# Optimization experiments

Hardware: AMD Instinct MI355X
Metric: run time of the kernel (lower is better)

The kernel has to match this reference:

```python
import jax, jax.numpy as jnp
import numpy as np

B, H, W, F, D = 8, 126, 126, 64, 32
ITERS, NIT = 3, 20
RHO, NU, DT, FRC = 1.0, 0.1, 0.1, 1.0
DX = 2.0 / (B + 1)
DY = 2.0 / (H + 1)
DX2, DY2 = DX * DX, DY * DY
DEN = 2.0 * (DX2 + DY2)


def _b_term(du_dx, dv_dy, du_dy, dv_dx):
    return RHO * ((du_dx + dv_dy) / DT - du_dx**2 - 2.0 * du_dy * dv_dx - dv_dy**2)


def build_b(u, v):
    b = jnp.zeros_like(u)
    # interior
    b = b.at[:, 1:-1, 1:-1].set(_b_term(
        (u[:, 1:-1, 2:] - u[:, 1:-1, :-2]) / (2 * DX),
        (v[:, 2:, 1:-1] - v[:, :-2, 1:-1]) / (2 * DY),
        (u[:, 2:, 1:-1] - u[:, :-2, 1:-1]) / (2 * DY),
        (v[:, 1:-1, 2:] - v[:, 1:-1, :-2]) / (2 * DX)))
    # periodic wrap, last column
    b = b.at[:, 1:-1, -1].set(_b_term(
        (u[:, 1:-1, 0] - u[:, 1:-1, -2]) / (2 * DX),
        (v[:, 2:, -1] - v[:, :-2, -1]) / (2 * DY),
        (u[:, 2:, -1] - u[:, :-2, -1]) / (2 * DY),
        (v[:, 1:-1, 0] - v[:, 1:-1, -2]) / (2 * DX)))
    # periodic wrap, first column
    b = b.at[:, 1:-1, 0].set(_b_term(
        (u[:, 1:-1, 1] - u[:, 1:-1, -1]) / (2 * DX),
        (v[:, 2:, 0] - v[:, :-2, 0]) / (2 * DY),
        (u[:, 2:, 0] - u[:, :-2, 0]) / (2 * DY),
        (v[:, 1:-1, 1] - v[:, 1:-1, -1]) / (2 * DX)))
    return b


def pressure_poisson(p, b):
    c = DX2 * DY2 / DEN

    def step(p, _):
        pn = p
        p = p.at[:, 1:-1, 1:-1].set(
            ((pn[:, 1:-1, 2:] + pn[:, 1:-1, :-2]) * DY2 + (pn[:, 2:, 1:-1] + pn[:, :-2, 1:-1]) * DX2) / DEN
            - c * b[:, 1:-1, 1:-1])
        p = p.at[:, 1:-1, -1].set(
            ((pn[:, 1:-1, 0] + pn[:, 1:-1, -2]) * DY2 + (pn[:, 2:, -1] + pn[:, :-2, -1]) * DX2) / DEN
            - c * b[:, 1:-1, -1])
        p = p.at[:, 1:-1, 0].set(
            ((pn[:, 1:-1, 1] + pn[:, 1:-1, -1]) * DY2 + (pn[:, 2:, 0] + pn[:, :-2, 0]) * DX2) / DEN
            - c * b[:, 1:-1, 0])
        # Neumann-style row boundaries (copy from updated p, as in torch code)
        p = p.at[:, -1].set(p[:, -2])
        p = p.at[:, 0].set(p[:, 1])
        return p, None

    p, _ = jax.lax.scan(step, p, None, length=NIT)
    return p


def velocity_step(u, v, p):
    un, vn = u, v
    uc = un[:, 1:-1, 1:-1]
    vc = vn[:, 1:-1, 1:-1]
    u_i = (uc - uc * DT / DX * (uc - un[:, 1:-1, :-2]) - vc * DT / DY * (uc - un[:, :-2, 1:-1])
           - DT / (2 * RHO * DX) * (p[:, 1:-1, 2:] - p[:, 1:-1, :-2])
           + NU * (DT / DX2 * (un[:, 1:-1, 2:] - 2 * uc + un[:, 1:-1, :-2])
                   + DT / DY2 * (un[:, 2:, 1:-1] - 2 * uc + un[:, :-2, 1:-1]))
           + FRC * DT)
    v_i = (vc - uc * DT / DX * (vc - vn[:, 1:-1, :-2]) - vc * DT / DY * (vc - vn[:, :-2, 1:-1])
           - DT / (2 * RHO * DY) * (p[:, 2:, 1:-1] - p[:, :-2, 1:-1])
           + NU * (DT / DX2 * (vn[:, 1:-1, 2:] - 2 * vc + vn[:, 1:-1, :-2])
                   + DT / DY2 * (vn[:, 2:, 1:-1] - 2 * vc + vn[:, :-2, 1:-1])))
    ue = un[:, 1:-1, -1]
    ve = vn[:, 1:-1, -1]
    u_e = (ue - ue * DT / DX * (ue - un[:, 1:-1, -2]) - ve * DT / DY * (ue - un[:, :-2, -1])
           - DT / (2 * RHO * DX) * (p[:, 1:-1, 0] - p[:, 1:-1, -2])
           + NU * (DT / DX2 * (un[:, 1:-1, 0] - 2 * ue + un[:, 1:-1, -2])
                   + DT / DY2 * (un[:, 2:, -1] - 2 * ue + un[:, :-2, -1]))
           + FRC * DT)
    v_e = (ve - ue * DT / DX * (ve - vn[:, 1:-1, -2]) - ve * DT / DY * (ve - vn[:, :-2, -1])
           - DT / (2 * RHO * DY) * (p[:, 2:, -1] - p[:, :-2, -1])
           + NU * (DT / DX2 * (vn[:, 1:-1, 0] - 2 * ve + vn[:, 1:-1, -2])
                   + DT / DY2 * (vn[:, 2:, -1] - 2 * ve + vn[:, :-2, -1])))
    u0c = un[:, 1:-1, 0]
    v0c = vn[:, 1:-1, 0]
    u_0 = (u0c - u0c * DT / DX * (u0c - un[:, 1:-1, -1]) - v0c * DT / DY * (u0c - un[:, :-2, 0])
           - DT / (2 * RHO * DX) * (p[:, 1:-1, 1] - p[:, 1:-1, -1])
           + NU * (DT / DX2 * (un[:, 1:-1, 1] - 2 * u0c + un[:, 1:-1, -1])
                   + DT / DY2 * (un[:, 2:, 0] - 2 * u0c + un[:, :-2, 0]))
           + FRC * DT)
    v_0 = (v0c - u0c * DT / DX * (v0c - vn[:, 1:-1, -1]) - v0c * DT / DY * (v0c - vn[:, :-2, 0])
           - DT / (2 * RHO * DY) * (p[:, 2:, 0] - p[:, :-2, 0])
           + NU * (DT / DX2 * (vn[:, 1:-1, 1] - 2 * v0c + vn[:, 1:-1, -1])
                   + DT / DY2 * (vn[:, 2:, 0] - 2 * v0c + vn[:, :-2, 0])))
    u = un.at[:, 1:-1, 1:-1].set(u_i).at[:, 1:-1, -1].set(u_e).at[:, 1:-1, 0].set(u_0)
    v = vn.at[:, 1:-1, 1:-1].set(v_i).at[:, 1:-1, -1].set(v_e).at[:, 1:-1, 0].set(v_0)
    u = u.at[:, 0].set(0.0).at[:, -1].set(0.0)
    v = v.at[:, 0].set(0.0).at[:, -1].set(0.0)
    return u, v


def setup_inputs() -> dict:
    key = jax.random.key(0)
    ks = jax.random.split(key, 5)
    x = jax.random.normal(ks[0], (B, H, W, F), jnp.float32) * 0.05
    u0 = jax.random.normal(ks[1], (B, H + 2, W + 2, D), jnp.float32) * 0.05
    v0 = jax.random.normal(ks[2], (B, H + 2, W + 2, D), jnp.float32) * 0.05
    w = jax.random.normal(ks[3], (D, F), jnp.float32) / np.float32(np.sqrt(F))
    b_lin = jax.random.normal(ks[4], (D,), jnp.float32) * 0.01
    return {"x": x, "u0": u0, "v0": v0, "w": w, "b_lin": b_lin}


def reference(x, u0, v0, w, b_lin):
    # pad spatial dims by 1 then linear preprocess: (B,H+2,W+2,F) -> (B,H+2,W+2,D)
    p = jnp.pad(x, ((0, 0), (1, 1), (1, 1), (0, 0)))
    p = jnp.einsum('bhwf,df->bhwd', p, w) + b_lin
    u, v = u0, v0
    for _ in range(ITERS):
        b = build_b(u, v)
        p = pressure_poisson(p, b)
        u, v = velocity_step(u, v, p)
    return p[:, -1, :, :]  # (B, W+2, D)
```

## Files before the change

### kernel.cpp

```cpp
#include <hip/hip_runtime.h>

#define NITER 20
#define OUTER 3

constexpr double DXd  = 2.0 / 9.0;
constexpr double DYd  = 2.0 / 127.0;
constexpr double DX2d = DXd * DXd;
constexpr double DY2d = DYd * DYd;
constexpr double DENd = 2.0 * (DX2d + DY2d);

constexpr float K1     = (float)(DY2d / DENd);
constexpr float K2     = (float)(DX2d / DENd);
constexpr float CC     = (float)(DX2d * DY2d / DENd);
constexpr float INV2DX = (float)(1.0 / (2.0 * DXd));
constexpr float INV2DY = (float)(1.0 / (2.0 * DYd));
constexpr float INVDT  = (float)(1.0 / 0.1);
constexpr float DTDX   = (float)(0.1 / DXd);
constexpr float DTDY   = (float)(0.1 / DYd);
constexpr float PGX    = (float)(0.1 / (2.0 * 1.0 * DXd));
constexpr float PGY    = (float)(0.1 / (2.0 * 1.0 * DYd));
constexpr float A1     = (float)(0.1 / DX2d);
constexpr float A2     = (float)(0.1 / DY2d);
constexpr float NUf    = 0.1f;
constexpr float FDT    = 0.1f;

__device__ __forceinline__ float bperm(int srcByte, float v) {
    return __int_as_float(__builtin_amdgcn_ds_bpermute(srcByte, __float_as_int(v)));
}

__global__ __launch_bounds__(256) void einsum_kernel(
    const float* __restrict__ x, const float* __restrict__ w,
    const float* __restrict__ bl, float* __restrict__ p0)
{
    int id = blockIdx.x * 256 + threadIdx.x;
    int c = id & 127, r = (id >> 7) & 127, b = id >> 14;
    float acc[32];
#pragma unroll
    for (int d = 0; d < 32; ++d) acc[d] = bl[d];
    if (r >= 1 && r <= 126 && c >= 1 && c <= 126) {
        const float* xp = x + (((size_t)(b * 126 + (r - 1))) * 126 + (c - 1)) * 64;
#pragma unroll
        for (int f = 0; f < 64; f += 4) {
            float4 xv = *(const float4*)(xp + f);
#pragma unroll
            for (int d = 0; d < 32; ++d) {
                acc[d] += xv.x * w[d * 64 + f] + xv.y * w[d * 64 + f + 1]
                        + xv.z * w[d * 64 + f + 2] + xv.w * w[d * 64 + f + 3];
            }
        }
    }
    float* op = p0 + ((size_t)b * 32) * 16384 + r * 128 + c;
#pragma unroll
    for (int d = 0; d < 32; ++d) op[(size_t)d * 16384] = acc[d];
}

__global__ __launch_bounds__(512, 2) void sim_kernel(
    const float* __restrict__ u0, const float* __restrict__ v0,
    const float* __restrict__ p0ws, const float* __restrict__ x,
    const float* __restrict__ w, const float* __restrict__ bl,
    float* __restrict__ out, int use_ws)
{
    __shared__ float sP[2][16][2][128];
    __shared__ float sU[16][2][128];
    __shared__ float sV[16][2][128];

    const int tid = threadIdx.x;
    const int tx = tid & 31, ty = tid >> 5;
    const int c0 = tx << 2, r0 = ty << 3;
    const int lane = tid & 63;
    const int srcL = (((lane & 32) | ((lane + 31) & 31)) << 2);
    const int srcR = (((lane & 32) | ((lane + 1) & 31)) << 2);
    const int bb = blockIdx.x & 7;
    const int d  = blockIdx.x >> 3;

    float pC[8][4], uC[8][4], vC[8][4], cb[8][4];

#pragma unroll
    for (int r = 0; r < 8; ++r) {
        const size_t base = ((size_t)((bb * 128 + (r0 + r)) * 128 + c0)) * 32 + d;
#pragma unroll
        for (int c = 0; c < 4; ++c) {
            uC[r][c] = u0[base + (size_t)c * 32];
            vC[r][c] = v0[base + (size_t)c * 32];
        }
    }

    if (use_ws) {
        const float* pp = p0ws + ((size_t)(bb * 32 + d)) * 16384;
#pragma unroll
        for (int r = 0; r < 8; ++r) {
            float4 t = *(const float4*)(pp + (r0 + r) * 128 + c0);
            pC[r][0] = t.x; pC[r][1] = t.y; pC[r][2] = t.z; pC[r][3] = t.w;
        }
    } else {
        const float blv = bl[d];
#pragma unroll
        for (int r = 0; r < 8; ++r) {
            const int gr = r0 + r;
#pragma unroll
            for (int c = 0; c < 4; ++c) {
                const int gc = c0 + c;
                float acc = blv;
                if (gr >= 1 && gr <= 126 && gc >= 1 && gc <= 126) {
                    const float* xp = x + (((size_t)(bb * 126 + (gr - 1))) * 126 + (gc - 1)) * 64;
                    for (int f = 0; f < 64; f += 4) {
                        float4 xv = *(const float4*)(xp + f);
                        acc += xv.x * w[d * 64 + f] + xv.y * w[d * 64 + f + 1]
                             + xv.z * w[d * 64 + f + 2] + xv.w * w[d * 64 + f + 3];
                    }
                }
                pC[r][c] = acc;
            }
        }
    }

    int s = 0;
    *(float4*)&sP[0][ty][0][c0] = make_float4(pC[0][0], pC[0][1], pC[0][2], pC[0][3]);
    *(float4*)&sP[0][ty][1][c0] = make_float4(pC[7][0], pC[7][1], pC[7][2], pC[7][3]);
    *(float4*)&sU[ty][0][c0]    = make_float4(uC[0][0], uC[0][1], uC[0][2], uC[0][3]);
    *(float4*)&sU[ty][1][c0]    = make_float4(uC[7][0], uC[7][1], uC[7][2], uC[7][3]);
    *(float4*)&sV[ty][0][c0]    = make_float4(vC[0][0], vC[0][1], vC[0][2], vC[0][3]);
    *(float4*)&sV[ty][1][c0]    = make_float4(vC[7][0], vC[7][1], vC[7][2], vC[7][3]);
    __syncthreads();

    const int tyN = (ty > 0) ? ty - 1 : 0;
    const int tyS = (ty < 15) ? ty + 1 : 15;

    for (int outer = 0; outer < OUTER; ++outer) {
        {
            float4 uN4 = *(const float4*)&sU[tyN][1][c0];
            float4 uS4 = *(const float4*)&sU[tyS][0][c0];
            float4 vN4 = *(const float4*)&sV[tyN][1][c0];
            float4 vS4 = *(const float4*)&sV[tyS][0][c0];
            float uNh[4] = {uN4.x, uN4.y, uN4.z, uN4.w};
            float uSh[4] = {uS4.x, uS4.y, uS4.z, uS4.w};
            float vNh[4] = {vN4.x, vN4.y, vN4.z, vN4.w};
            float vSh[4] = {vS4.x, vS4.y, vS4.z, vS4.w};
#pragma unroll
            for (int r = 0; r < 8; ++r) {
                const int gr = r0 + r;
                const bool valid = (gr >= 1) && (gr <= 126);
                float uWh = bperm(srcL, uC[r][3]);
                float uEh = bperm(srcR, uC[r][0]);
                float vWh = bperm(srcL, vC[r][3]);
                float vEh = bperm(srcR, vC[r][0]);
#pragma unroll
                for (int c = 0; c < 4; ++c) {
                    float uE = (c < 3) ? uC[r][c + 1] : uEh;
                    float uW = (c > 0) ? uC[r][c - 1] : uWh;
                    float vE = (c < 3) ? vC[r][c + 1] : vEh;
                    float vW = (c > 0) ? vC[r][c - 1] : vWh;
                    float uN = (r > 0) ? uC[r - 1][c] : uNh[c];
                    float uS = (r < 7) ? uC[r + 1][c] : uSh[c];
                    float vN = (r > 0) ? vC[r - 1][c] : vNh[c];
                    float vS = (r < 7) ? vC[r + 1][c] : vSh[c];
                    float dudx = (uE - uW) * INV2DX;
                    float dvdy = (vS - vN) * INV2DY;
                    float dudy = (uS - uN) * INV2DY;
                    float dvdx = (vE - vW) * INV2DX;
                    float bt = (dudx + dvdy) * INVDT - dudx * dudx
                             - 2.0f * dudy * dvdx - dvdy * dvdy;
                    cb[r][c] = valid ? CC * bt : 0.0f;
                }
            }
        }

        for (int it = 0; it < NITER; ++it) {
            float4 t4 = *(const float4*)&sP[s][tyN][1][c0];
            float4 b4 = *(const float4*)&sP[s][tyS][0][c0];
            float nrow[4] = {t4.x, t4.y, t4.z, t4.w};
            float shalo[4] = {b4.x, b4.y, b4.z, b4.w};
#pragma unroll
            for (int r = 0; r < 8; ++r) {
                const int gr = r0 + r;
                const bool valid = (gr >= 1) && (gr <= 126);
                float old0[4];
#pragma unroll
                for (int c = 0; c < 4; ++c) old0[c] = pC[r][c];
                float pWh = bperm(srcL, old0[3]);
                float pEh = bperm(srcR, old0[0]);
#pragma unroll
                for (int c = 0; c < 4; ++c) {
                    float E = (c < 3) ? old0[c + 1] : pEh;
                    float W = (c > 0) ? old0[c - 1] : pWh;
                    float N = nrow[c];
                    float S = (r < 7) ? pC[r + 1][c] : shalo[c];
                    float nv = (E + W) * K1 + (N + S) * K2 - cb[r][c];
                    pC[r][c] = valid ? nv : old0[c];
                }
#pragma unroll
                for (int c = 0; c < 4; ++c) nrow[c] = old0[c];
            }
            if (ty == 0) {
#pragma unroll
                for (int c = 0; c < 4; ++c) pC[0][c] = pC[1][c];
            }
            if (ty == 15) {
#pragma unroll
                for (int c = 0; c < 4; ++c) pC[7][c] = pC[6][c];
            }
            *(float4*)&sP[s ^ 1][ty][0][c0] = make_float4(pC[0][0], pC[0][1], pC[0][2], pC[0][3]);
            *(float4*)&sP[s ^ 1][ty][1][c0] = make_float4(pC[7][0], pC[7][1], pC[7][2], pC[7][3]);
            __syncthreads();
            s ^= 1;
        }

        {
            float4 ut4 = *(const float4*)&sU[tyN][1][c0];
            float4 us4 = *(const float4*)&sU[tyS][0][c0];
            float4 vt4 = *(const float4*)&sV[tyN][1][c0];
            float4 vs4 = *(const float4*)&sV[tyS][0][c0];
            float4 pt4 = *(const float4*)&sP[s][tyN][1][c0];
            float4 pb4 = *(const float4*)&sP[s][tyS][0][c0];
            float uNh[4] = {ut4.x, ut4.y, ut4.z, ut4.w};
            float uSh[4] = {us4.x, us4.y, us4.z, us4.w};
            float vNh[4] = {vt4.x, vt4.y, vt4.z, vt4.w};
            float vSh[4] = {vs4.x, vs4.y, vs4.z, vs4.w};
            float pNh[4] = {pt4.x, pt4.y, pt4.z, pt4.w};
            float pSh[4] = {pb4.x, pb4.y, pb4.z, pb4.w};
            __syncthreads();

            float uNrow[4], vNrow[4];
#pragma unroll
            for (int c = 0; c < 4; ++c) { uNrow[c] = uNh[c]; vNrow[c] = vNh[c]; }
#pragma unroll
            for (int r = 0; r < 8; ++r) {
                const int gr = r0 + r;
                const bool valid = (gr >= 1) && (gr <= 126);
                float uold[4], vold[4];
#pragma unroll
                for (int c = 0; c < 4; ++c) { uold[c] = uC[r][c]; vold[c] = vC[r][c]; }
                float uWh = bperm(srcL, uold[3]);
                float uEh = bperm(srcR, uold[0]);
                float vWh = bperm(srcL, vold[3]);
                float vEh = bperm(srcR, vold[0]);
                float pWh = bperm(srcL, pC[r][3]);
                float pEh = bperm(srcR, pC[r][0]);
#pragma unroll
                for (int c = 0; c < 4; ++c) {
                    float uc = uold[c], vc = vold[c];
                    float uE = (c < 3) ? uold[c + 1] : uEh;
                    float uW = (c > 0) ? uold[c - 1] : uWh;
                    float vE = (c < 3) ? vold[c + 1] : vEh;
                    float vW = (c > 0) ? vold[c - 1] : vWh;
                    float uN = uNrow[c];
                    float uS = (r < 7) ? uC[r + 1][c] : uSh[c];
                    float vN = vNrow[c];
                    float vS = (r < 7) ? vC[r + 1][c] : vSh[c];
                    float pE = (c < 3) ? pC[r][c + 1] : pEh;
                    float pW = (c > 0) ? pC[r][c - 1] : pWh;
                    float pN = (r > 0) ? pC[r - 1][c] : pNh[c];
                    float pS = (r < 7) ? pC[r + 1][c] : pSh[c];

                    float unew = uc - uc * DTDX * (uc - uW) - vc * DTDY * (uc - uN)
                               - PGX * (pE - pW)
                               + NUf * (A1 * (uE - 2.0f * uc + uW) + A2 * (uS - 2.0f * uc + uN))
                               + FDT;
                    float vnew = vc - uc * DTDX * (vc - vW) - vc * DTDY * (vc - vN)
                               - PGY * (pS - pN)
                               + NUf * (A1 * (vE - 2.0f * vc + vW) + A2 * (vS - 2.0f * vc + vN));
                    uC[r][c] = valid ? unew : uc;
                    vC[r][c] = valid ? vnew : vc;
                }
#pragma unroll
                for (int c = 0; c < 4; ++c) { uNrow[c] = uold[c]; vNrow[c] = vold[c]; }
            }
            if (ty == 0) {
#pragma unroll
                for (int c = 0; c < 4; ++c) { uC[0][c] = 0.0f; vC[0][c] = 0.0f; }
            }
            if (ty == 15) {
#pragma unroll
                for (int c = 0; c < 4; ++c) { uC[7][c] = 0.0f; vC[7][c] = 0.0f; }
            }
            *(float4*)&sU[ty][0][c0] = make_float4(uC[0][0], uC[0][1], uC[0][2], uC[0][3]);
            *(float4*)&sU[ty][1][c0] = make_float4(uC[7][0], uC[7][1], uC[7][2], uC[7][3]);
            *(float4*)&sV[ty][0][c0] = make_float4(vC[0][0], vC[0][1], vC[0][2], vC[0][3]);
            *(float4*)&sV[ty][1][c0] = make_float4(vC[7][0], vC[7][1], vC[7][2], vC[7][3]);
            __syncthreads();
        }
    }

    if (ty == 15) {
        float* op = out + ((size_t)bb * 128 + c0) * 32 + d;
        op[0]  = pC[7][0];
        op[32] = pC[7][1];
        op[64] = pC[7][2];
        op[96] = pC[7][3];
    }
}

extern "C" void kernel_launch(void* const* d_in, const int* in_sizes, int n_in,
                              void* d_out, int out_size, void* d_ws, size_t ws_size,
                              hipStream_t stream) {
    const float* x  = (const float*)d_in[0];
    const float* u0 = (const float*)d_in[1];
    const float* v0 = (const float*)d_in[2];
    const float* w  = (const float*)d_in[3];
    const float* bl = (const float*)d_in[4];
    float* out = (float*)d_out;
    float* p0  = (float*)d_ws;

    const size_t need = (size_t)8 * 32 * 128 * 128 * sizeof(float);
    const int use_ws = (ws_size >= need) ? 1 : 0;

    if (use_ws) {
        einsum_kernel<<<512, 256, 0, stream>>>(x, w, bl, p0);
    }
    sim_kernel<<<256, 512, 0, stream>>>(u0, v0, p0, x, w, bl, out, use_ws);
}
```

Baseline: 268.8 us.

## Double threads per block, halve rows per thread, skip final velocity update

Each block now runs 1024 threads, and each thread owns a 4x4 tile instead of 8x4. This raises the number of waves per CU and shortens each thread's serial dependency chain in the Jacobi sweeps. The separate P/U/V shared arrays become one reused buffer. The validity masks are dropped because boundary rows are overwritten anyway. The last outer iteration's velocity update is skipped since the output depends only on pressure. The trade-off is more threads at each barrier, extra syncs to reuse the shared buffer, and a relative increase in halo exchange traffic.

```diff
diff --git a/kernel.cpp b/kernel.cpp
--- a/kernel.cpp
+++ b/kernel.cpp
@@ -54,29 +54,29 @@
     for (int d = 0; d < 32; ++d) op[(size_t)d * 16384] = acc[d];
 }
 
-__global__ __launch_bounds__(512, 2) void sim_kernel(
+__global__ __launch_bounds__(1024, 4) void sim_kernel(
     const float* __restrict__ u0, const float* __restrict__ v0,
     const float* __restrict__ p0ws, const float* __restrict__ x,
     const float* __restrict__ w, const float* __restrict__ bl,
     float* __restrict__ out, int use_ws)
 {
-    __shared__ float sP[2][16][2][128];
-    __shared__ float sU[16][2][128];
-    __shared__ float sV[16][2][128];
+    __shared__ float S[32][4][128];
 
     const int tid = threadIdx.x;
     const int tx = tid & 31, ty = tid >> 5;
-    const int c0 = tx << 2, r0 = ty << 3;
+    const int c0 = tx << 2, r0 = ty << 2;
     const int lane = tid & 63;
     const int srcL = (((lane & 32) | ((lane + 31) & 31)) << 2);
     const int srcR = (((lane & 32) | ((lane + 1) & 31)) << 2);
     const int bb = blockIdx.x & 7;
     const int d  = blockIdx.x >> 3;
-
-    float pC[8][4], uC[8][4], vC[8][4], cb[8][4];
-
-#pragma unroll
-    for (int r = 0; r < 8; ++r) {
+    const int tyN = (ty > 0) ? ty - 1 : 0;
+    const int tyS = (ty < 31) ? ty + 1 : 31;
+
+    float pC[4][4], uC[4][4], vC[4][4], cb[4][4];
+
+#pragma unroll
+    for (int r = 0; r < 4; ++r) {
         const size_t base = ((size_t)((bb * 128 + (r0 + r)) * 128 + c0)) * 32 + d;
 #pragma unroll
         for (int c = 0; c < 4; ++c) {
@@ -88,14 +88,14 @@
     if (use_ws) {
         const float* pp = p0ws + ((size_t)(bb * 32 + d)) * 16384;
 #pragma unroll
-        for (int r = 0; r < 8; ++r) {
+        for (int r = 0; r < 4; ++r) {
             float4 t = *(const float4*)(pp + (r0 + r) * 128 + c0);
             pC[r][0] = t.x; pC[r][1] = t.y; pC[r][2] = t.z; pC[r][3] = t.w;
         }
     } else {
         const float blv = bl[d];
 #pragma unroll
-        for (int r = 0; r < 8; ++r) {
+        for (int r = 0; r < 4; ++r) {
             const int gr = r0 + r;
 #pragma unroll
             for (int c = 0; c < 4; ++c) {
@@ -114,79 +114,77 @@
         }
     }
 
-    int s = 0;
-    *(float4*)&sP[0][ty][0][c0] = make_float4(pC[0][0], pC[0][1], pC[0][2], pC[0][3]);
-    *(float4*)&sP[0][ty][1][c0] = make_float4(pC[7][0], pC[7][1], pC[7][2], pC[7][3]);
-    *(float4*)&sU[ty][0][c0]    = make_float4(uC[0][0], uC[0][1], uC[0][2], uC[0][3]);
-    *(float4*)&sU[ty][1][c0]    = make_float4(uC[7][0], uC[7][1], uC[7][2], uC[7][3]);
-    *(float4*)&sV[ty][0][c0]    = make_float4(vC[0][0], vC[0][1], vC[0][2], vC[0][3]);
-    *(float4*)&sV[ty][1][c0]    = make_float4(vC[7][0], vC[7][1], vC[7][2], vC[7][3]);
+    *(float4*)&S[ty][0][c0] = make_float4(uC[0][0], uC[0][1], uC[0][2], uC[0][3]);
+    *(float4*)&S[ty][1][c0] = make_float4(uC[3][0], uC[3][1], uC[3][2], uC[3][3]);
+    *(float4*)&S[ty][2][c0] = make_float4(vC[0][0], vC[0][1], vC[0][2], vC[0][3]);
+    *(float4*)&S[ty][3][c0] = make_float4(vC[3][0], vC[3][1], vC[3][2], vC[3][3]);
     __syncthreads();
 
-    const int tyN = (ty > 0) ? ty - 1 : 0;
-    const int tyS = (ty < 15) ? ty + 1 : 15;
-
     for (int outer = 0; outer < OUTER; ++outer) {
-        {
-            float4 uN4 = *(const float4*)&sU[tyN][1][c0];
-            float4 uS4 = *(const float4*)&sU[tyS][0][c0];
-            float4 vN4 = *(const float4*)&sV[tyN][1][c0];
-            float4 vS4 = *(const float4*)&sV[tyS][0][c0];
-            float uNh[4] = {uN4.x, uN4.y, uN4.z, uN4.w};
-            float uSh[4] = {uS4.x, uS4.y, uS4.z, uS4.w};
-            float vNh[4] = {vN4.x, vN4.y, vN4.z, vN4.w};
-            float vSh[4] = {vS4.x, vS4.y, vS4.z, vS4.w};
-#pragma unroll
-            for (int r = 0; r < 8; ++r) {
-                const int gr = r0 + r;
-                const bool valid = (gr >= 1) && (gr <= 126);
-                float uWh = bperm(srcL, uC[r][3]);
-                float uEh = bperm(srcR, uC[r][0]);
-                float vWh = bperm(srcL, vC[r][3]);
-                float vEh = bperm(srcR, vC[r][0]);
-#pragma unroll
-                for (int c = 0; c < 4; ++c) {
-                    float uE = (c < 3) ? uC[r][c + 1] : uEh;
-                    float uW = (c > 0) ? uC[r][c - 1] : uWh;
-                    float vE = (c < 3) ? vC[r][c + 1] : vEh;
-                    float vW = (c > 0) ? vC[r][c - 1] : vWh;
-                    float uN = (r > 0) ? uC[r - 1][c] : uNh[c];
-                    float uS = (r < 7) ? uC[r + 1][c] : uSh[c];
-                    float vN = (r > 0) ? vC[r - 1][c] : vNh[c];
-                    float vS = (r < 7) ? vC[r + 1][c] : vSh[c];
-                    float dudx = (uE - uW) * INV2DX;
-                    float dvdy = (vS - vN) * INV2DY;
-                    float dudy = (uS - uN) * INV2DY;
-                    float dvdx = (vE - vW) * INV2DX;
-                    float bt = (dudx + dvdy) * INVDT - dudx * dudx
-                             - 2.0f * dudy * dvdx - dvdy * dvdy;
-                    cb[r][c] = valid ? CC * bt : 0.0f;
-                }
-            }
-        }
+        float4 uN4 = *(const float4*)&S[tyN][1][c0];
+        float4 uS4 = *(const float4*)&S[tyS][0][c0];
+        float4 vN4 = *(const float4*)&S[tyN][3][c0];
+        float4 vS4 = *(const float4*)&S[tyS][2][c0];
+        float uNh[4] = {uN4.x, uN4.y, uN4.z, uN4.w};
+        float uSh[4] = {uS4.x, uS4.y, uS4.z, uS4.w};
+        float vNh[4] = {vN4.x, vN4.y, vN4.z, vN4.w};
+        float vSh[4] = {vS4.x, vS4.y, vS4.z, vS4.w};
+
+#pragma unroll
+        for (int r = 0; r < 4; ++r) {
+            float uWh = bperm(srcL, uC[r][3]);
+            float uEh = bperm(srcR, uC[r][0]);
+            float vWh = bperm(srcL, vC[r][3]);
+            float vEh = bperm(srcR, vC[r][0]);
+#pragma unroll
+            for (int c = 0; c < 4; ++c) {
+                float uE = (c < 3) ? uC[r][c + 1] : uEh;
+                float uW = (c > 0) ? uC[r][c - 1] : uWh;
+                float vE = (c < 3) ? vC[r][c + 1] : vEh;
+                float vW = (c > 0) ? vC[r][c - 1] : vWh;
+                float uN = (r > 0) ? uC[r - 1][c] : uNh[c];
+                float uS_ = (r < 3) ? uC[r + 1][c] : uSh[c];
+                float vN = (r > 0) ? vC[r - 1][c] : vNh[c];
+                float vS_ = (r < 3) ? vC[r + 1][c] : vSh[c];
+                float dudx = (uE - uW) * INV2DX;
+                float dvdy = (vS_ - vN) * INV2DY;
+                float dudy = (uS_ - uN) * INV2DY;
+                float dvdx = (vE - vW) * INV2DX;
+                float bt = (dudx + dvdy) * INVDT - dudx * dudx
+                         - 2.0f * dudy * dvdx - dvdy * dvdy;
+                cb[r][c] = CC * bt;
+            }
+        }
+        __syncthreads();
+        *(float4*)&S[ty][0][c0] = make_float4(pC[0][0], pC[0][1], pC[0][2], pC[0][3]);
+        *(float4*)&S[ty][1][c0] = make_float4(pC[3][0], pC[3][1], pC[3][2], pC[3][3]);
+        __syncthreads();
 
         for (int it = 0; it < NITER; ++it) {
-            float4 t4 = *(const float4*)&sP[s][tyN][1][c0];
-            float4 b4 = *(const float4*)&sP[s][tyS][0][c0];
+            const int rb = (it & 1) << 1;
+            const int wb = rb ^ 2;
+            float4 t4 = *(const float4*)&S[tyN][rb + 1][c0];
+            float4 b4 = *(const float4*)&S[tyS][rb + 0][c0];
             float nrow[4] = {t4.x, t4.y, t4.z, t4.w};
             float shalo[4] = {b4.x, b4.y, b4.z, b4.w};
-#pragma unroll
-            for (int r = 0; r < 8; ++r) {
-                const int gr = r0 + r;
-                const bool valid = (gr >= 1) && (gr <= 126);
+            float pWh[4], pEh[4];
+#pragma unroll
+            for (int r = 0; r < 4; ++r) {
+                pWh[r] = bperm(srcL, pC[r][3]);
+                pEh[r] = bperm(srcR, pC[r][0]);
+            }
+#pragma unroll
+            for (int r = 0; r < 4; ++r) {
                 float old0[4];
 #pragma unroll
                 for (int c = 0; c < 4; ++c) old0[c] = pC[r][c];
-                float pWh = bperm(srcL, old0[3]);
-                float pEh = bperm(srcR, old0[0]);
 #pragma unroll
                 for (int c = 0; c < 4; ++c) {
-                    float E = (c < 3) ? old0[c + 1] : pEh;
-                    float W = (c > 0) ? old0[c - 1] : pWh;
+                    float E = (c < 3) ? old0[c + 1] : pEh[r];
+                    float W = (c > 0) ? old0[c - 1] : pWh[r];
                     float N = nrow[c];
-                    float S = (r < 7) ? pC[r + 1][c] : shalo[c];
-                    float nv = (E + W) * K1 + (N + S) * K2 - cb[r][c];
-                    pC[r][c] = valid ? nv : old0[c];
+                    float Sv = (r < 3) ? pC[r + 1][c] : shalo[c];
+                    pC[r][c] = (E + W) * K1 + (N + Sv) * K2 - cb[r][c];
                 }
 #pragma unroll
                 for (int c = 0; c < 4; ++c) nrow[c] = old0[c];
@@ -195,38 +193,26 @@
 #pragma unroll
                 for (int c = 0; c < 4; ++c) pC[0][c] = pC[1][c];
             }
-            if (ty == 15) {
-#pragma unroll
-                for (int c = 0; c < 4; ++c) pC[7][c] = pC[6][c];
-            }
-            *(float4*)&sP[s ^ 1][ty][0][c0] = make_float4(pC[0][0], pC[0][1], pC[0][2], pC[0][3]);
-            *(float4*)&sP[s ^ 1][ty][1][c0] = make_float4(pC[7][0], pC[7][1], pC[7][2], pC[7][3]);
+            if (ty == 31) {
+#pragma unroll
+                for (int c = 0; c < 4; ++c) pC[3][c] = pC[2][c];
+            }
+            *(float4*)&S[ty][wb][c0]     = make_float4(pC[0][0], pC[0][1], pC[0][2], pC[0][3]);
+            *(float4*)&S[ty][wb + 1][c0] = make_float4(pC[3][0], pC[3][1], pC[3][2], pC[3][3]);
             __syncthreads();
-            s ^= 1;
-        }
-
-        {
-            float4 ut4 = *(const float4*)&sU[tyN][1][c0];
-            float4 us4 = *(const float4*)&sU[tyS][0][c0];
-            float4 vt4 = *(const float4*)&sV[tyN][1][c0];
-            float4 vs4 = *(const float4*)&sV[tyS][0][c0];
-            float4 pt4 = *(const float4*)&sP[s][tyN][1][c0];
-            float4 pb4 = *(const float4*)&sP[s][tyS][0][c0];
-            float uNh[4] = {ut4.x, ut4.y, ut4.z, ut4.w};
-            float uSh[4] = {us4.x, us4.y, us4.z, us4.w};
-            float vNh[4] = {vt4.x, vt4.y, vt4.z, vt4.w};
-            float vSh[4] = {vs4.x, vs4.y, vs4.z, vs4.w};
+        }
+
+        if (outer < OUTER - 1) {
+            float4 pt4 = *(const float4*)&S[tyN][1][c0];
+            float4 pb4 = *(const float4*)&S[tyS][0][c0];
             float pNh[4] = {pt4.x, pt4.y, pt4.z, pt4.w};
             float pSh[4] = {pb4.x, pb4.y, pb4.z, pb4.w};
-            __syncthreads();
 
             float uNrow[4], vNrow[4];
 #pragma unroll
             for (int c = 0; c < 4; ++c) { uNrow[c] = uNh[c]; vNrow[c] = vNh[c]; }
 #pragma unroll
-            for (int r = 0; r < 8; ++r) {
-                const int gr = r0 + r;
-                const bool valid = (gr >= 1) && (gr <= 126);
+            for (int r = 0; r < 4; ++r) {
                 float uold[4], vold[4];
 #pragma unroll
                 for (int c = 0; c < 4; ++c) { uold[c] = uC[r][c]; vold[c] = vC[r][c]; }
@@ -244,23 +230,23 @@
                     float vE = (c < 3) ? vold[c + 1] : vEh;
                     float vW = (c > 0) ? vold[c - 1] : vWh;
                     float uN = uNrow[c];
-                    float uS = (r < 7) ? uC[r + 1][c] : uSh[c];
+                    float uS_ = (r < 3) ? uC[r + 1][c] : uSh[c];
                     float vN = vNrow[c];
-                    float vS = (r < 7) ? vC[r + 1][c] : vSh[c];
+                    float vS_ = (r < 3) ? vC[r + 1][c] : vSh[c];
                     float pE = (c < 3) ? pC[r][c + 1] : pEh;
                     float pW = (c > 0) ? pC[r][c - 1] : pWh;
                     float pN = (r > 0) ? pC[r - 1][c] : pNh[c];
-                    float pS = (r < 7) ? pC[r + 1][c] : pSh[c];
+                    float pS = (r < 3) ? pC[r + 1][c] : pSh[c];
 
                     float unew = uc - uc * DTDX * (uc - uW) - vc * DTDY * (uc - uN)
                                - PGX * (pE - pW)
-                               + NUf * (A1 * (uE - 2.0f * uc + uW) + A2 * (uS - 2.0f * uc + uN))
+                               + NUf * (A1 * (uE - 2.0f * uc + uW) + A2 * (uS_ - 2.0f * uc + uN))
                                + FDT;
                     float vnew = vc - uc * DTDX * (vc - vW) - vc * DTDY * (vc - vN)
                                - PGY * (pS - pN)
-                               + NUf * (A1 * (vE - 2.0f * vc + vW) + A2 * (vS - 2.0f * vc + vN));
-                    uC[r][c] = valid ? unew : uc;
-                    vC[r][c] = valid ? vnew : vc;
+                               + NUf * (A1 * (vE - 2.0f * vc + vW) + A2 * (vS_ - 2.0f * vc + vN));
+                    uC[r][c] = unew;
+                    vC[r][c] = vnew;
                 }
 #pragma unroll
                 for (int c = 0; c < 4; ++c) { uNrow[c] = uold[c]; vNrow[c] = vold[c]; }
@@ -269,24 +255,25 @@
 #pragma unroll
                 for (int c = 0; c < 4; ++c) { uC[0][c] = 0.0f; vC[0][c] = 0.0f; }
             }
-            if (ty == 15) {
-#pragma unroll
-                for (int c = 0; c < 4; ++c) { uC[7][c] = 0.0f; vC[7][c] = 0.0f; }
-            }
-            *(float4*)&sU[ty][0][c0] = make_float4(uC[0][0], uC[0][1], uC[0][2], uC[0][3]);
-            *(float4*)&sU[ty][1][c0] = make_float4(uC[7][0], uC[7][1], uC[7][2], uC[7][3]);
-            *(float4*)&sV[ty][0][c0] = make_float4(vC[0][0], vC[0][1], vC[0][2], vC[0][3]);
-            *(float4*)&sV[ty][1][c0] = make_float4(vC[7][0], vC[7][1], vC[7][2], vC[7][3]);
+            if (ty == 31) {
+#pragma unroll
+                for (int c = 0; c < 4; ++c) { uC[3][c] = 0.0f; vC[3][c] = 0.0f; }
+            }
             __syncthreads();
-        }
-    }
-
-    if (ty == 15) {
+            *(float4*)&S[ty][0][c0] = make_float4(uC[0][0], uC[0][1], uC[0][2], uC[0][3]);
+            *(float4*)&S[ty][1][c0] = make_float4(uC[3][0], uC[3][1], uC[3][2], uC[3][3]);
+            *(float4*)&S[ty][2][c0] = make_float4(vC[0][0], vC[0][1], vC[0][2], vC[0][3]);
+            *(float4*)&S[ty][3][c0] = make_float4(vC[3][0], vC[3][1], vC[3][2], vC[3][3]);
+            __syncthreads();
+        }
+    }
+
+    if (ty == 31) {
         float* op = out + ((size_t)bb * 128 + c0) * 32 + d;
-        op[0]  = pC[7][0];
-        op[32] = pC[7][1];
-        op[64] = pC[7][2];
-        op[96] = pC[7][3];
+        op[0]  = pC[3][0];
+        op[32] = pC[3][1];
+        op[64] = pC[3][2];
+        op[96] = pC[3][3];
     }
 }
 
@@ -307,5 +294,5 @@
     if (use_ws) {
         einsum_kernel<<<512, 256, 0, stream>>>(x, w, bl, p0);
     }
-    sim_kernel<<<256, 512, 0, stream>>>(u0, v0, p0, x, w, bl, out, use_ws);
-}
+    sim_kernel<<<256, 1024, 0, stream>>>(u0, v0, p0, x, w, bl, out, use_ws);
+}
```

After: 287.7 us. +7.0%, slower.
